# Optimization experiments

Measured on AMD Instinct MI355X. Metric: run time of the kernel, lower is better.

Reference implementation:

```python
import jax, jax.numpy as jnp
import numpy as np

D_MODEL = 1024
N_HEADS = 16
D_K = D_MODEL // N_HEADS


def setup_inputs() -> dict:
    key = jax.random.key(0)
    kx, kq, kk, kv, ko = jax.random.split(key, 5)
    scale = 1.0 / np.sqrt(D_MODEL)
    return {
        "x": jax.random.normal(kx, (2, 2048, D_MODEL), dtype=jnp.float32),
        "W_Q": jax.random.normal(kq, (D_MODEL, D_MODEL), dtype=jnp.float32) * scale,
        "W_K": jax.random.normal(kk, (D_MODEL, D_MODEL), dtype=jnp.float32) * scale,
        "W_V": jax.random.normal(kv, (D_MODEL, D_MODEL), dtype=jnp.float32) * scale,
        "W_O": jax.random.normal(ko, (D_MODEL, D_MODEL), dtype=jnp.float32) * scale,
    }


def reference(x, W_Q, W_K, W_V, W_O) -> jnp.ndarray:
    B, S, _ = x.shape
    # Projections; weights stored as (d_model, d_model), applied as x @ W (Linear weight transposed convention folded into init)
    def heads(w):
        return jnp.einsum('bsd,de->bse', x, w).reshape(B, S, N_HEADS, D_K).transpose(0, 2, 1, 3)
    Q, K, V = heads(W_Q), heads(W_K), heads(W_V)  # (B,H,S,d_k)
    scores = jnp.einsum('bhqd,bhkd->bhqk', Q, K) / jnp.sqrt(jnp.asarray(D_K, x.dtype))
    causal_mask = jnp.triu(jnp.ones((S, S), dtype=bool), k=1)  # True above diagonal
    scores = jnp.where(causal_mask[None, None], jnp.asarray(-jnp.inf, x.dtype), scores)
    attn = jax.nn.softmax(scores, axis=-1)
    out = jnp.einsum('bhqk,bhkd->bhqd', attn, V)  # (B,H,S,d_k)
    out = out.transpose(0, 2, 1, 3).reshape(B, S, N_HEADS * D_K)
    return jnp.einsum('bsd,de->bse', out, W_O)
```

## Files before the change

### kernel.cpp

```cpp
#include <hip/hip_runtime.h>

typedef unsigned short u16;
typedef unsigned int u32;
typedef __attribute__((ext_vector_type(8))) __bf16 bf16x8;
typedef __attribute__((ext_vector_type(2))) __bf16 bf16x2;
typedef __attribute__((ext_vector_type(4))) float f32x4;
typedef __attribute__((ext_vector_type(16))) float f32x16;
typedef __attribute__((ext_vector_type(4))) u32 u32x4;

__device__ inline u16 f2bf(float f) {
  unsigned u = __builtin_bit_cast(unsigned, f);
  u += 0x7FFFu + ((u >> 16) & 1u);
  return (u16)(u >> 16);
}

__device__ inline u32 packbf(float a, float b) {
  bf16x2 t;
  t[0] = (__bf16)a;
  t[1] = (__bf16)b;
  return __builtin_bit_cast(u32, t);
}

__device__ inline void async16(const void* g, void* l) {
  __builtin_amdgcn_global_load_lds((const __attribute__((address_space(1))) void*)g,
                                   (__attribute__((address_space(3))) void*)l, 16, 0, 0);
}

__global__ __launch_bounds__(256) void prep(const float* __restrict__ x, u16* __restrict__ xb,
                                            const float* __restrict__ W0,
                                            const float* __restrict__ W1,
                                            const float* __restrict__ W2,
                                            const float* __restrict__ W3,
                                            u16* __restrict__ WtQKV,
                                            u16* __restrict__ WtO) {
  const int z = blockIdx.z;
  if (z == 4) {
    const int base = (blockIdx.y * 32 + blockIdx.x) * 4 * 256 + threadIdx.x;
#pragma unroll
    for (int it = 0; it < 4; ++it) {
      const int i = base + it * 256;
      float4 v = ((const float4*)x)[i];
      ushort4 r;
      r.x = f2bf(v.x); r.y = f2bf(v.y); r.z = f2bf(v.z); r.w = f2bf(v.w);
      ((ushort4*)xb)[i] = r;
    }
    return;
  }
  __shared__ u16 tile[32][33];
  const float* W = (z == 0) ? W0 : (z == 1) ? W1 : (z == 2) ? W2 : W3;
  u16* Wt = (z < 3) ? (WtQKV + (size_t)z * 1024 * 1024) : WtO;
  const float s = (z == 0) ? 0.18033688011112042f : 1.0f;
  const int e0 = blockIdx.x * 32;
  const int d0 = blockIdx.y * 32;
  const int tx = threadIdx.x & 31;
  const int ty = threadIdx.x >> 5;
#pragma unroll
  for (int i = ty; i < 32; i += 8)
    tile[i][tx] = f2bf(W[(size_t)(d0 + i) * 1024 + e0 + tx] * s);
  __syncthreads();
#pragma unroll
  for (int i = ty; i < 32; i += 8)
    Wt[(size_t)(e0 + i) * 1024 + d0 + tx] = tile[tx][i];
}

template <int OUT_BF16, int FUSE_V>
__global__ __launch_bounds__(256) void gemm_bt(const u16* __restrict__ A,
                                               const u16* __restrict__ Bt,
                                               void* __restrict__ Cp,
                                               u16* __restrict__ Vtg,
                                               int M, int N, int K) {
  __shared__ __align__(16) u16 As[128 * 32];
  __shared__ __align__(16) u16 Bs[128 * 32];
  const int tid = threadIdx.x;
  const int lane = tid & 63;
  const int wave = tid >> 6;
  const int lr = lane & 15;
  const int lk = (lane >> 4) * 8;
  const int wm = (wave >> 1) * 64;
  const int wn = (wave & 1) * 64;

  const int flat = blockIdx.y * gridDim.x + blockIdx.x;
  const int chunk = (gridDim.x * gridDim.y) >> 3;
  const int nf = (flat & 7) * chunk + (flat >> 3);
  const int bm = (nf % gridDim.x) * 128;
  const int bn = (nf / gridDim.x) * 128;

  const int srow = lane >> 2;
  const int scol = (lane & 3) * 8;

  f32x4 acc[4][4] = {};

  for (int k0 = 0; k0 < K; k0 += 32) {
#pragma unroll
    for (int r = 0; r < 2; ++r) {
      const int chnk = r * 4 + wave;
      const int row = chnk * 16 + srow;
      async16(A + (size_t)(bm + row) * K + k0 + scol, &As[chnk * 512 + lane * 8]);
      async16(Bt + (size_t)(bn + row) * K + k0 + scol, &Bs[chnk * 512 + lane * 8]);
    }
    __syncthreads();
    bf16x8 a[4], b[4];
#pragma unroll
    for (int i = 0; i < 4; ++i) {
      a[i] = *(const bf16x8*)&As[(wm + i * 16 + lr) * 32 + lk];
      b[i] = *(const bf16x8*)&Bs[(wn + i * 16 + lr) * 32 + lk];
    }
#pragma unroll
    for (int mi = 0; mi < 4; ++mi)
#pragma unroll
      for (int ni = 0; ni < 4; ++ni)
        acc[mi][ni] = __builtin_amdgcn_mfma_f32_16x16x32_bf16(a[mi], b[ni], acc[mi][ni], 0, 0, 0);
    __syncthreads();
  }

#pragma unroll
  for (int mi = 0; mi < 4; ++mi) {
    const int row = bm + wm + mi * 16 + (lane >> 4) * 4;
#pragma unroll
    for (int ni = 0; ni < 4; ++ni) {
      const int col = bn + wn + ni * 16 + lr;
#pragma unroll
      for (int j = 0; j < 4; ++j) {
        if (OUT_BF16)
          ((u16*)Cp)[(size_t)(row + j) * N + col] = f2bf(acc[mi][ni][j]);
        else
          ((float*)Cp)[(size_t)(row + j) * N + col] = acc[mi][ni][j];
      }
      if (FUSE_V && col >= 2048) {
        const int bloc = row >> 11;
        const int s = row & 2047;
        const int sp = (s & ~12) | ((s & 4) << 1) | ((s & 8) >> 1);
        ushort4 v4;
        v4.x = f2bf(acc[mi][ni][0]);
        v4.y = f2bf(acc[mi][ni][1]);
        v4.z = f2bf(acc[mi][ni][2]);
        v4.w = f2bf(acc[mi][ni][3]);
        *(ushort4*)(Vtg + (size_t)(bloc * 1024 + (col - 2048)) * 2048 + sp) = v4;
      }
    }
  }
}

__global__ __launch_bounds__(256, 2) void attn_kernel(const u16* __restrict__ QKV,
                                                      const u16* __restrict__ Vtg,
                                                      u16* __restrict__ Opart,
                                                      float* __restrict__ Lpart) {
  constexpr int S = 2048, LD = 3072;
  constexpr float MFIX = 12.0f;
  __shared__ __align__(16) u16 Ks[2][64 * 64];
  __shared__ __align__(16) u16 Vs[2][64 * 64];

  const int flat = blockIdx.y * 16 + blockIdx.x;
  const int nf = (flat & 7) * 64 + (flat >> 3);
  const int xi = nf & 15;
  const int bh = nf >> 4;

  const int g = 7 - (xi >> 1);
  const int c = xi & 1;
  const int b = bh >> 4, h = bh & 15;
  const int tid = threadIdx.x, lane = tid & 63, w = tid >> 6;
  const int l31 = lane & 31, lh = lane >> 5;

  const int qbase = g * 256 + w * 64;
  const int ktlast = 4 * g + w;
  const int ktbeg = c * (2 * g + 2);
  const int ktend = (c + 1) * (2 * g + 2);

  bf16x8 qf[2][4];
#pragma unroll
  for (int qh = 0; qh < 2; ++qh) {
    const u16* qrow = QKV + (size_t)(b * S + qbase + qh * 32 + l31) * LD + h * 64;
#pragma unroll
    for (int cc = 0; cc < 4; ++cc) qf[qh][cc] = *(const bf16x8*)(qrow + cc * 16 + lh * 8);
  }

  const int c0 = tid, c1 = tid + 256;
  const int r0 = c0 >> 3, x0 = ((c0 & 7) ^ (r0 & 7)) << 3;
  const int r1 = c1 >> 3, x1 = ((c1 & 7) ^ (r1 & 7)) << 3;
  const u16* Kbase = QKV + (size_t)b * S * LD + 1024 + h * 64;
  const u16* Vbase = Vtg + (size_t)bh * 64 * 2048;

#define STAGE(buf, kt_)                                                          \
  do {                                                                           \
    async16(Kbase + (size_t)((kt_)*64 + r0) * LD + x0, &Ks[buf][c0 * 8]);        \
    async16(Kbase + (size_t)((kt_)*64 + r1) * LD + x1, &Ks[buf][c1 * 8]);        \
    async16(Vbase + (size_t)r0 * 2048 + (kt_)*64 + x0, &Vs[buf][c0 * 8]);        \
    async16(Vbase + (size_t)r1 * 2048 + (kt_)*64 + x1, &Vs[buf][c1 * 8]);        \
  } while (0)

  f32x16 o00 = {}, o01 = {}, o10 = {}, o11 = {};
  float l0 = 0.f, l1 = 0.f;

#define TREE16(dst, arr)                                                         \
  do {                                                                           \
    float v_[16];                                                                \
    _Pragma("unroll") for (int r_ = 0; r_ < 16; ++r_) v_[r_] = (arr)[r_];        \
    _Pragma("unroll") for (int s_ = 8; s_ >= 1; s_ >>= 1)                        \
      _Pragma("unroll") for (int r_ = 0; r_ < s_; ++r_) v_[r_] += v_[r_ + s_];   \
    dst += v_[0];                                                                \
  } while (0)

#define MAKE_PA(pa, pk, q4)                                                      \
  bf16x8 pa;                                                                     \
  {                                                                              \
    u32x4 wv_;                                                                   \
    wv_[0] = (pk)[(q4) + 0];                                                     \
    wv_[1] = (pk)[(q4) + 1];                                                     \
    wv_[2] = (pk)[(q4) + 2];                                                     \
    wv_[3] = (pk)[(q4) + 3];                                                     \
    pa = __builtin_bit_cast(bf16x8, wv_);                                        \
  }

  STAGE(0, ktbeg);

  int cur = 0;
  for (int kt = ktbeg; kt < ktend; ++kt) {
    if (kt + 1 < ktend) {
      STAGE(cur ^ 1, kt + 1);
      asm volatile("s_waitcnt vmcnt(4)" ::: "memory");
    } else {
      asm volatile("s_waitcnt vmcnt(0)" ::: "memory");
    }
    __builtin_amdgcn_s_barrier();
    __builtin_amdgcn_sched_barrier(0);

    const bool active = (kt <= ktlast);
    if (active) {
      const bool full = (kt < ktlast);
      const u16* ks = Ks[cur];
      const u16* vs = Vs[cur];

      f32x16 t00 = {}, t10 = {}, t01 = {}, t11 = {};
      __builtin_amdgcn_s_setprio(1);
#pragma unroll
      for (int cc = 0; cc < 4; ++cc) {
        const int ci = 2 * cc + lh;
        const bf16x8 kf0 = *(const bf16x8*)&ks[l31 * 64 + ((ci ^ (l31 & 7)) << 3)];
        const bf16x8 kf1 = *(const bf16x8*)&ks[(32 + l31) * 64 + ((ci ^ (l31 & 7)) << 3)];
        t00 = __builtin_amdgcn_mfma_f32_32x32x16_bf16(kf0, qf[0][cc], t00, 0, 0, 0);
        t01 = __builtin_amdgcn_mfma_f32_32x32x16_bf16(kf0, qf[1][cc], t01, 0, 0, 0);
        if (full) t10 = __builtin_amdgcn_mfma_f32_32x32x16_bf16(kf1, qf[0][cc], t10, 0, 0, 0);
        t11 = __builtin_amdgcn_mfma_f32_32x32x16_bf16(kf1, qf[1][cc], t11, 0, 0, 0);
      }
      __builtin_amdgcn_s_setprio(0);

      if (!full) {
#pragma unroll
        for (int r = 0; r < 16; ++r) {
          const int ko = (r & 3) + 8 * (r >> 2) + 4 * lh;
          if (ko > l31) { t00[r] = -3e38f; t11[r] = -3e38f; }
        }
      }

      u32 pk0[8], pk1[8];

#pragma unroll
      for (int r = 0; r < 16; ++r) t00[r] = exp2f(t00[r] - MFIX);
#pragma unroll
      for (int r = 0; r < 16; ++r) t01[r] = exp2f(t01[r] - MFIX);
      TREE16(l0, t00);
      TREE16(l1, t01);
#pragma unroll
      for (int j = 0; j < 8; ++j) {
        pk0[j] = packbf(t00[2 * j], t00[2 * j + 1]);
        pk1[j] = packbf(t01[2 * j], t01[2 * j + 1]);
      }
      __builtin_amdgcn_s_setprio(1);
#pragma unroll
      for (int kc = 0; kc < 2; ++kc) {
        const int q4 = kc * 4;
        MAKE_PA(pa0, pk0, q4)
        MAKE_PA(pa1, pk1, q4)
        const int ci = 2 * kc + lh;
        const bf16x8 vd0 = *(const bf16x8*)&vs[l31 * 64 + ((ci ^ (l31 & 7)) << 3)];
        const bf16x8 vd1 = *(const bf16x8*)&vs[(32 + l31) * 64 + ((ci ^ (l31 & 7)) << 3)];
        o00 = __builtin_amdgcn_mfma_f32_32x32x16_bf16(pa0, vd0, o00, 0, 0, 0);
        o01 = __builtin_amdgcn_mfma_f32_32x32x16_bf16(pa0, vd1, o01, 0, 0, 0);
        o10 = __builtin_amdgcn_mfma_f32_32x32x16_bf16(pa1, vd0, o10, 0, 0, 0);
        o11 = __builtin_amdgcn_mfma_f32_32x32x16_bf16(pa1, vd1, o11, 0, 0, 0);
      }
      __builtin_amdgcn_s_setprio(0);

      if (full) {
#pragma unroll
        for (int r = 0; r < 16; ++r) t10[r] = exp2f(t10[r] - MFIX);
        TREE16(l0, t10);
#pragma unroll
        for (int j = 0; j < 8; ++j) pk0[j] = packbf(t10[2 * j], t10[2 * j + 1]);
      }
#pragma unroll
      for (int r = 0; r < 16; ++r) t11[r] = exp2f(t11[r] - MFIX);
      TREE16(l1, t11);
#pragma unroll
      for (int j = 0; j < 8; ++j) pk1[j] = packbf(t11[2 * j], t11[2 * j + 1]);

      __builtin_amdgcn_s_setprio(1);
#pragma unroll
      for (int kc = 0; kc < 2; ++kc) {
        const int q4 = kc * 4;
        MAKE_PA(pa1, pk1, q4)
        const int ci = 2 * (kc + 2) + lh;
        const bf16x8 vd0 = *(const bf16x8*)&vs[l31 * 64 + ((ci ^ (l31 & 7)) << 3)];
        const bf16x8 vd1 = *(const bf16x8*)&vs[(32 + l31) * 64 + ((ci ^ (l31 & 7)) << 3)];
        if (full) {
          MAKE_PA(pa0, pk0, q4)
          o00 = __builtin_amdgcn_mfma_f32_32x32x16_bf16(pa0, vd0, o00, 0, 0, 0);
          o01 = __builtin_amdgcn_mfma_f32_32x32x16_bf16(pa0, vd1, o01, 0, 0, 0);
        }
        o10 = __builtin_amdgcn_mfma_f32_32x32x16_bf16(pa1, vd0, o10, 0, 0, 0);
        o11 = __builtin_amdgcn_mfma_f32_32x32x16_bf16(pa1, vd1, o11, 0, 0, 0);
      }
      __builtin_amdgcn_s_setprio(0);
    }

    asm volatile("s_waitcnt lgkmcnt(0)" ::: "memory");
    __builtin_amdgcn_s_barrier();
    cur ^= 1;
  }
#undef STAGE
#undef TREE16
#undef MAKE_PA

  const float l0t = l0 + __shfl_xor(l0, 32);
  const float l1t = l1 + __shfl_xor(l1, 32);
  u16* Oc = Opart + (size_t)c * 4096 * 1024;
#pragma unroll
  for (int r = 0; r < 16; ++r) {
    const int qo = (r & 3) + 8 * (r >> 2) + 4 * lh;
    u16* p0 = Oc + (size_t)(b * S + qbase + qo) * 1024 + h * 64 + l31;
    u16* p1 = p0 + (size_t)32 * 1024;
    p0[0] = f2bf(o00[r]);
    p0[32] = f2bf(o01[r]);
    p1[0] = f2bf(o10[r]);
    p1[32] = f2bf(o11[r]);
  }
  if (lh == 0) {
    Lpart[(size_t)c * 4096 * 16 + (size_t)(b * S + qbase + l31) * 16 + h] = l0t;
    Lpart[(size_t)c * 4096 * 16 + (size_t)(b * S + qbase + 32 + l31) * 16 + h] = l1t;
  }
}

__global__ __launch_bounds__(256) void combine(const u16* __restrict__ Opart,
                                               const float* __restrict__ Lpart,
                                               u16* __restrict__ Obuf) {
  const int i = blockIdx.x * 256 + threadIdx.x;
  const int row = i >> 7;
  const int cw = (i & 127) * 8;
  const int h = cw >> 6;
  const float l = Lpart[(size_t)row * 16 + h] + Lpart[(size_t)4096 * 16 + (size_t)row * 16 + h];
  const float inv = 1.0f / l;
  const bf16x8 a = *(const bf16x8*)(Opart + (size_t)row * 1024 + cw);
  const bf16x8 bq = *(const bf16x8*)(Opart + (size_t)4096 * 1024 + (size_t)row * 1024 + cw);
  u16 out[8];
#pragma unroll
  for (int j = 0; j < 8; ++j) out[j] = f2bf(((float)a[j] + (float)bq[j]) * inv);
  *(uint4*)(Obuf + (size_t)row * 1024 + cw) = *(uint4*)out;
}

extern "C" void kernel_launch(void* const* d_in, const int* in_sizes, int n_in,
                              void* d_out, int out_size, void* d_ws, size_t ws_size,
                              hipStream_t stream) {
  const float* x  = (const float*)d_in[0];
  const float* WQ = (const float*)d_in[1];
  const float* WK = (const float*)d_in[2];
  const float* WV = (const float*)d_in[3];
  const float* WO = (const float*)d_in[4];
  float* out = (float*)d_out;

  u16* xb    = (u16*)d_ws;
  u16* WtQKV = xb + (size_t)4096 * 1024;
  u16* WtO   = WtQKV + (size_t)3072 * 1024;
  u16* QKV   = WtO + (size_t)1024 * 1024;
  u16* Obuf  = QKV + (size_t)4096 * 3072;
  u16* Vtg   = Obuf + (size_t)4096 * 1024;
  u16* Opart = Vtg + (size_t)2048 * 2048;
  float* Lpart = (float*)(Opart + (size_t)2 * 4096 * 1024);

  prep<<<dim3(32, 32, 5), 256, 0, stream>>>(x, xb, WQ, WK, WV, WO, WtQKV, WtO);

  gemm_bt<1, 1><<<dim3(32, 24), 256, 0, stream>>>(xb, WtQKV, QKV, Vtg, 4096, 3072, 1024);
  attn_kernel<<<dim3(16, 32), 256, 0, stream>>>(QKV, Vtg, Opart, Lpart);
  combine<<<2048, 256, 0, stream>>>(Opart, Lpart, Obuf);
  gemm_bt<0, 0><<<dim3(32, 8), 256, 0, stream>>>(Obuf, WtO, out, nullptr, 4096, 1024, 1024);
}
```

Baseline: 138.2 us.

## Add 256x256-tile 8-wave QKV GEMM with split-K double buffering; fold softmax offset

Replaces the 128x128 QKV projection GEMM with a new 512-thread kernel using 256x256 output tiles, 64-wide K steps split into two 32-wide halves, double-buffered async LDS loads with swizzling, and interleaved A/B staging across barriers. The larger tile raises reuse per loaded byte and reduces block count to 192. The attention kernel also initialises score accumulators to -MFIX so the subtraction before exp2 is dropped. The cost is more registers and LDS per block, a grid that covers fewer blocks than there are CUs, and hardcoded shape constants.

After: 140.5 us. No clear change (+1.6%).

```diff
diff --git a/kernel.cpp b/kernel.cpp
--- a/kernel.cpp
+++ b/kernel.cpp
@@ -63,11 +63,136 @@
     Wt[(size_t)(e0 + i) * 1024 + d0 + tx] = tile[tx][i];
 }
 
-template <int OUT_BF16, int FUSE_V>
+__global__ __launch_bounds__(512, 2) void gemm8(const u16* __restrict__ A,
+                                                const u16* __restrict__ Bt,
+                                                u16* __restrict__ C,
+                                                u16* __restrict__ Vtg) {
+  constexpr int K = 1024, N = 3072, NT = 16;
+  __shared__ __align__(16) u16 Als[2][2][128 * 64];
+  __shared__ __align__(16) u16 Bls[2][2][128 * 64];
+
+  const int tid = threadIdx.x;
+  const int lane = tid & 63;
+  const int wid = tid >> 6;
+  const int wm = wid >> 2;
+  const int wn = wid & 3;
+  const int lr = lane & 15;
+  const int kc4 = lane >> 4;
+
+  const int flat = blockIdx.y * gridDim.x + blockIdx.x;
+  const int nf = (flat & 7) * 24 + (flat >> 3);
+  const int bm = (nf % 16) * 256;
+  const int bn = (nf / 16) * 256;
+
+  int srow[2], skof[2], sdst[2];
+#pragma unroll
+  for (int i = 0; i < 2; ++i) {
+    const int ch = tid + 512 * i;
+    const int R = ch >> 3, c = ch & 7;
+    const int cp = c ^ (R & 7);
+    srow[i] = 2 * R + (cp >> 2);
+    skof[i] = (cp & 3) * 8;
+    sdst[i] = ch * 8;
+  }
+
+#define STAGEH(LDSA, G, rowbase, o, kap, kt_)                                          \
+  do {                                                                                 \
+    _Pragma("unroll") for (int i_ = 0; i_ < 2; ++i_)                                   \
+      async16(G + (size_t)((rowbase) + srow[i_]) * K + (kt_)*64 + (kap)*32 + skof[i_], \
+              &LDSA[o][kap][sdst[i_]]);                                                \
+  } while (0)
+
+#define FRAG_OFF(r) ((((r) >> 1) * 8 + ((((r)&1) * 4 + kc4) ^ (((r) >> 1) & 7))) * 8)
+
+  f32x4 acc[8][4] = {};
+  bf16x8 af[4], bf[4];
+
+  STAGEH(Als, A, bm, 0, 0, 0);
+  STAGEH(Bls, Bt, bn, 0, 0, 0);
+  STAGEH(Als, A, bm, 0, 1, 0);
+  STAGEH(Bls, Bt, bn, 0, 1, 0);
+
+  for (int kt = 0; kt < NT; ++kt) {
+    const int s = kt & 1, o = s ^ 1;
+    const bool more = (kt + 1 < NT);
+
+#pragma unroll
+    for (int kk = 0; kk < 2; ++kk) {
+      if (more) STAGEH(Als, A, bm, o, kk, kt + 1);
+      if (more) {
+        asm volatile("s_waitcnt vmcnt(6)" ::: "memory");
+      } else if (kk == 0) {
+        asm volatile("s_waitcnt vmcnt(4)" ::: "memory");
+      } else {
+        asm volatile("s_waitcnt vmcnt(0)" ::: "memory");
+      }
+      __builtin_amdgcn_s_barrier();
+      __builtin_amdgcn_sched_barrier(0);
+
+#pragma unroll
+      for (int ni = 0; ni < 4; ++ni)
+        bf[ni] = *(const bf16x8*)&Bls[s][kk][FRAG_OFF(wn * 64 + ni * 16 + lr)];
+#pragma unroll
+      for (int mi = 0; mi < 4; ++mi)
+        af[mi] = *(const bf16x8*)&Als[s][kk][FRAG_OFF(wm * 128 + mi * 16 + lr)];
+      asm volatile("s_waitcnt lgkmcnt(0)" ::: "memory");
+      __builtin_amdgcn_sched_barrier(0);
+      __builtin_amdgcn_s_setprio(1);
+#pragma unroll
+      for (int mi = 0; mi < 4; ++mi)
+#pragma unroll
+        for (int ni = 0; ni < 4; ++ni)
+          acc[mi][ni] = __builtin_amdgcn_mfma_f32_16x16x32_bf16(af[mi], bf[ni], acc[mi][ni], 0, 0, 0);
+      __builtin_amdgcn_s_setprio(0);
+      __builtin_amdgcn_s_barrier();
+
+      if (more) STAGEH(Bls, Bt, bn, o, kk, kt + 1);
+#pragma unroll
+      for (int mi = 0; mi < 4; ++mi)
+        af[mi] = *(const bf16x8*)&Als[s][kk][FRAG_OFF(wm * 128 + (mi + 4) * 16 + lr)];
+      asm volatile("s_waitcnt lgkmcnt(0)" ::: "memory");
+      __builtin_amdgcn_sched_barrier(0);
+      __builtin_amdgcn_s_setprio(1);
+#pragma unroll
+      for (int mi = 0; mi < 4; ++mi)
+#pragma unroll
+        for (int ni = 0; ni < 4; ++ni)
+          acc[mi + 4][ni] = __builtin_amdgcn_mfma_f32_16x16x32_bf16(af[mi], bf[ni], acc[mi + 4][ni], 0, 0, 0);
+      __builtin_amdgcn_s_setprio(0);
+      __builtin_amdgcn_s_barrier();
+    }
+  }
+#undef STAGEH
+#undef FRAG_OFF
+
+#pragma unroll
+  for (int mi = 0; mi < 8; ++mi) {
+    const int row = bm + wm * 128 + mi * 16 + (lane >> 4) * 4;
+#pragma unroll
+    for (int ni = 0; ni < 4; ++ni) {
+      const int col = bn + wn * 64 + ni * 16 + lr;
+#pragma unroll
+      for (int j = 0; j < 4; ++j)
+        C[(size_t)(row + j) * N + col] = f2bf(acc[mi][ni][j]);
+      if (col >= 2048) {
+        const int bloc = row >> 11;
+        const int sidx = row & 2047;
+        const int sp = (sidx & ~12) | ((sidx & 4) << 1) | ((sidx & 8) >> 1);
+        ushort4 v4;
+        v4.x = f2bf(acc[mi][ni][0]);
+        v4.y = f2bf(acc[mi][ni][1]);
+        v4.z = f2bf(acc[mi][ni][2]);
+        v4.w = f2bf(acc[mi][ni][3]);
+        *(ushort4*)(Vtg + (size_t)(bloc * 1024 + (col - 2048)) * 2048 + sp) = v4;
+      }
+    }
+  }
+}
+
+template <int OUT_BF16>
 __global__ __launch_bounds__(256) void gemm_bt(const u16* __restrict__ A,
                                                const u16* __restrict__ Bt,
                                                void* __restrict__ Cp,
-                                               u16* __restrict__ Vtg,
                                                int M, int N, int K) {
   __shared__ __align__(16) u16 As[128 * 32];
   __shared__ __align__(16) u16 Bs[128 * 32];
@@ -126,17 +251,6 @@
         else
           ((float*)Cp)[(size_t)(row + j) * N + col] = acc[mi][ni][j];
       }
-      if (FUSE_V && col >= 2048) {
-        const int bloc = row >> 11;
-        const int s = row & 2047;
-        const int sp = (s & ~12) | ((s & 4) << 1) | ((s & 8) >> 1);
-        ushort4 v4;
-        v4.x = f2bf(acc[mi][ni][0]);
-        v4.y = f2bf(acc[mi][ni][1]);
-        v4.z = f2bf(acc[mi][ni][2]);
-        v4.w = f2bf(acc[mi][ni][3]);
-        *(ushort4*)(Vtg + (size_t)(bloc * 1024 + (col - 2048)) * 2048 + sp) = v4;
-      }
     }
   }
 }
@@ -230,7 +344,9 @@
       const u16* ks = Ks[cur];
       const u16* vs = Vs[cur];
 
-      f32x16 t00 = {}, t10 = {}, t01 = {}, t11 = {};
+      f32x16 t00, t10, t01, t11;
+#pragma unroll
+      for (int r = 0; r < 16; ++r) { t00[r] = -MFIX; t10[r] = -MFIX; t01[r] = -MFIX; t11[r] = -MFIX; }
       __builtin_amdgcn_s_setprio(1);
 #pragma unroll
       for (int cc = 0; cc < 4; ++cc) {
@@ -255,9 +371,9 @@
       u32 pk0[8], pk1[8];
 
 #pragma unroll
-      for (int r = 0; r < 16; ++r) t00[r] = exp2f(t00[r] - MFIX);
-#pragma unroll
-      for (int r = 0; r < 16; ++r) t01[r] = exp2f(t01[r] - MFIX);
+      for (int r = 0; r < 16; ++r) t00[r] = exp2f(t00[r]);
+#pragma unroll
+      for (int r = 0; r < 16; ++r) t01[r] = exp2f(t01[r]);
       TREE16(l0, t00);
       TREE16(l1, t01);
 #pragma unroll
@@ -283,13 +399,13 @@
 
       if (full) {
 #pragma unroll
-        for (int r = 0; r < 16; ++r) t10[r] = exp2f(t10[r] - MFIX);
+        for (int r = 0; r < 16; ++r) t10[r] = exp2f(t10[r]);
         TREE16(l0, t10);
 #pragma unroll
         for (int j = 0; j < 8; ++j) pk0[j] = packbf(t10[2 * j], t10[2 * j + 1]);
       }
 #pragma unroll
-      for (int r = 0; r < 16; ++r) t11[r] = exp2f(t11[r] - MFIX);
+      for (int r = 0; r < 16; ++r) t11[r] = exp2f(t11[r]);
       TREE16(l1, t11);
 #pragma unroll
       for (int j = 0; j < 8; ++j) pk1[j] = packbf(t11[2 * j], t11[2 * j + 1]);
@@ -378,8 +494,8 @@
 
   prep<<<dim3(32, 32, 5), 256, 0, stream>>>(x, xb, WQ, WK, WV, WO, WtQKV, WtO);
 
-  gemm_bt<1, 1><<<dim3(32, 24), 256, 0, stream>>>(xb, WtQKV, QKV, Vtg, 4096, 3072, 1024);
+  gemm8<<<dim3(16, 12), 512, 0, stream>>>(xb, WtQKV, QKV, Vtg);
   attn_kernel<<<dim3(16, 32), 256, 0, stream>>>(QKV, Vtg, Opart, Lpart);
   combine<<<2048, 256, 0, stream>>>(Opart, Lpart, Obuf);
-  gemm_bt<0, 0><<<dim3(32, 8), 256, 0, stream>>>(Obuf, WtO, out, nullptr, 4096, 1024, 1024);
-}
+  gemm_bt<0><<<dim3(32, 8), 256, 0, stream>>>(Obuf, WtO, out, 4096, 1024, 1024);
+}
```

## Fuse split-KV combine into output GEMM A-load and fold MFIX into accumulator init

Applied to the files above, without the earlier changes.

Drops the separate combine kernel. The output projection GEMM now reads both attention partial outputs and their row sums directly, normalises them and converts to bf16 while staging the A tile into LDS. This removes one launch and the Obuf round trip through memory. In exchange, every bn block repeats the combine work and the A loads become synchronous instead of async. Separately, the score accumulators start at -MFIX so the per-element subtraction before exp2 goes away.

After: 166.1 us. +20.2%, slower.

```diff
diff --git a/kernel.cpp b/kernel.cpp
--- a/kernel.cpp
+++ b/kernel.cpp
@@ -63,12 +63,11 @@
     Wt[(size_t)(e0 + i) * 1024 + d0 + tx] = tile[tx][i];
 }
 
-template <int OUT_BF16, int FUSE_V>
-__global__ __launch_bounds__(256) void gemm_bt(const u16* __restrict__ A,
-                                               const u16* __restrict__ Bt,
-                                               void* __restrict__ Cp,
-                                               u16* __restrict__ Vtg,
-                                               int M, int N, int K) {
+__global__ __launch_bounds__(256) void gemm_qkv(const u16* __restrict__ A,
+                                                const u16* __restrict__ Bt,
+                                                u16* __restrict__ C,
+                                                u16* __restrict__ Vtg) {
+  constexpr int K = 1024, N = 3072;
   __shared__ __align__(16) u16 As[128 * 32];
   __shared__ __align__(16) u16 Bs[128 * 32];
   const int tid = threadIdx.x;
@@ -120,13 +119,9 @@
     for (int ni = 0; ni < 4; ++ni) {
       const int col = bn + wn + ni * 16 + lr;
 #pragma unroll
-      for (int j = 0; j < 4; ++j) {
-        if (OUT_BF16)
-          ((u16*)Cp)[(size_t)(row + j) * N + col] = f2bf(acc[mi][ni][j]);
-        else
-          ((float*)Cp)[(size_t)(row + j) * N + col] = acc[mi][ni][j];
-      }
-      if (FUSE_V && col >= 2048) {
+      for (int j = 0; j < 4; ++j)
+        C[(size_t)(row + j) * N + col] = f2bf(acc[mi][ni][j]);
+      if (col >= 2048) {
         const int bloc = row >> 11;
         const int s = row & 2047;
         const int sp = (s & ~12) | ((s & 4) << 1) | ((s & 8) >> 1);
@@ -141,6 +136,76 @@
   }
 }
 
+__global__ __launch_bounds__(256) void gemm_out(const u16* __restrict__ Opart,
+                                                const float* __restrict__ Lpart,
+                                                const u16* __restrict__ Bt,
+                                                float* __restrict__ out) {
+  constexpr int K = 1024, N = 1024;
+  __shared__ __align__(16) u16 As[128 * 32];
+  __shared__ __align__(16) u16 Bs[128 * 32];
+  const int tid = threadIdx.x;
+  const int lane = tid & 63;
+  const int wave = tid >> 6;
+  const int lr = lane & 15;
+  const int lk = (lane >> 4) * 8;
+  const int wm = (wave >> 1) * 64;
+  const int wn = (wave & 1) * 64;
+
+  const int flat = blockIdx.y * gridDim.x + blockIdx.x;
+  const int chunk = (gridDim.x * gridDim.y) >> 3;
+  const int nf = (flat & 7) * chunk + (flat >> 3);
+  const int bm = (nf % gridDim.x) * 128;
+  const int bn = (nf / gridDim.x) * 128;
+
+  const int srow = lane >> 2;
+  const int scol = (lane & 3) * 8;
+
+  f32x4 acc[4][4] = {};
+
+  for (int k0 = 0; k0 < K; k0 += 32) {
+    const int hh = (k0 + scol) >> 6;
+#pragma unroll
+    for (int r = 0; r < 2; ++r) {
+      const int chnk = r * 4 + wave;
+      const int row = bm + chnk * 16 + srow;
+      const bf16x8 a0 = *(const bf16x8*)(Opart + (size_t)row * 1024 + k0 + scol);
+      const bf16x8 a1 = *(const bf16x8*)(Opart + (size_t)4096 * 1024 + (size_t)row * 1024 + k0 + scol);
+      const float inv = 1.0f / (Lpart[(size_t)row * 16 + hh] +
+                                Lpart[(size_t)4096 * 16 + (size_t)row * 16 + hh]);
+      u16 tmp[8];
+#pragma unroll
+      for (int j = 0; j < 8; ++j) tmp[j] = f2bf(((float)a0[j] + (float)a1[j]) * inv);
+      *(uint4*)&As[chnk * 512 + lane * 8] = *(uint4*)tmp;
+      async16(Bt + (size_t)(bn + chnk * 16 + srow) * K + k0 + scol, &Bs[chnk * 512 + lane * 8]);
+    }
+    __syncthreads();
+    bf16x8 a[4], b[4];
+#pragma unroll
+    for (int i = 0; i < 4; ++i) {
+      a[i] = *(const bf16x8*)&As[(wm + i * 16 + lr) * 32 + lk];
+      b[i] = *(const bf16x8*)&Bs[(wn + i * 16 + lr) * 32 + lk];
+    }
+#pragma unroll
+    for (int mi = 0; mi < 4; ++mi)
+#pragma unroll
+      for (int ni = 0; ni < 4; ++ni)
+        acc[mi][ni] = __builtin_amdgcn_mfma_f32_16x16x32_bf16(a[mi], b[ni], acc[mi][ni], 0, 0, 0);
+    __syncthreads();
+  }
+
+#pragma unroll
+  for (int mi = 0; mi < 4; ++mi) {
+    const int row = bm + wm + mi * 16 + (lane >> 4) * 4;
+#pragma unroll
+    for (int ni = 0; ni < 4; ++ni) {
+      const int col = bn + wn + ni * 16 + lr;
+#pragma unroll
+      for (int j = 0; j < 4; ++j)
+        out[(size_t)(row + j) * N + col] = acc[mi][ni][j];
+    }
+  }
+}
+
 __global__ __launch_bounds__(256, 2) void attn_kernel(const u16* __restrict__ QKV,
                                                       const u16* __restrict__ Vtg,
                                                       u16* __restrict__ Opart,
@@ -230,7 +295,9 @@
       const u16* ks = Ks[cur];
       const u16* vs = Vs[cur];
 
-      f32x16 t00 = {}, t10 = {}, t01 = {}, t11 = {};
+      f32x16 t00, t10, t01, t11;
+#pragma unroll
+      for (int r = 0; r < 16; ++r) { t00[r] = -MFIX; t10[r] = -MFIX; t01[r] = -MFIX; t11[r] = -MFIX; }
       __builtin_amdgcn_s_setprio(1);
 #pragma unroll
       for (int cc = 0; cc < 4; ++cc) {
@@ -255,9 +322,9 @@
       u32 pk0[8], pk1[8];
 
 #pragma unroll
-      for (int r = 0; r < 16; ++r) t00[r] = exp2f(t00[r] - MFIX);
-#pragma unroll
-      for (int r = 0; r < 16; ++r) t01[r] = exp2f(t01[r] - MFIX);
+      for (int r = 0; r < 16; ++r) t00[r] = exp2f(t00[r]);
+#pragma unroll
+      for (int r = 0; r < 16; ++r) t01[r] = exp2f(t01[r]);
       TREE16(l0, t00);
       TREE16(l1, t01);
 #pragma unroll
@@ -283,13 +350,13 @@
 
       if (full) {
 #pragma unroll
-        for (int r = 0; r < 16; ++r) t10[r] = exp2f(t10[r] - MFIX);
+        for (int r = 0; r < 16; ++r) t10[r] = exp2f(t10[r]);
         TREE16(l0, t10);
 #pragma unroll
         for (int j = 0; j < 8; ++j) pk0[j] = packbf(t10[2 * j], t10[2 * j + 1]);
       }
 #pragma unroll
-      for (int r = 0; r < 16; ++r) t11[r] = exp2f(t11[r] - MFIX);
+      for (int r = 0; r < 16; ++r) t11[r] = exp2f(t11[r]);
       TREE16(l1, t11);
 #pragma unroll
       for (int j = 0; j < 8; ++j) pk1[j] = packbf(t11[2 * j], t11[2 * j + 1]);
@@ -340,23 +407,6 @@
   }
 }
 
-__global__ __launch_bounds__(256) void combine(const u16* __restrict__ Opart,
-                                               const float* __restrict__ Lpart,
-                                               u16* __restrict__ Obuf) {
-  const int i = blockIdx.x * 256 + threadIdx.x;
-  const int row = i >> 7;
-  const int cw = (i & 127) * 8;
-  const int h = cw >> 6;
-  const float l = Lpart[(size_t)row * 16 + h] + Lpart[(size_t)4096 * 16 + (size_t)row * 16 + h];
-  const float inv = 1.0f / l;
-  const bf16x8 a = *(const bf16x8*)(Opart + (size_t)row * 1024 + cw);
-  const bf16x8 bq = *(const bf16x8*)(Opart + (size_t)4096 * 1024 + (size_t)row * 1024 + cw);
-  u16 out[8];
-#pragma unroll
-  for (int j = 0; j < 8; ++j) out[j] = f2bf(((float)a[j] + (float)bq[j]) * inv);
-  *(uint4*)(Obuf + (size_t)row * 1024 + cw) = *(uint4*)out;
-}
-
 extern "C" void kernel_launch(void* const* d_in, const int* in_sizes, int n_in,
                               void* d_out, int out_size, void* d_ws, size_t ws_size,
                               hipStream_t stream) {
@@ -371,15 +421,13 @@
   u16* WtQKV = xb + (size_t)4096 * 1024;
   u16* WtO   = WtQKV + (size_t)3072 * 1024;
   u16* QKV   = WtO + (size_t)1024 * 1024;
-  u16* Obuf  = QKV + (size_t)4096 * 3072;
-  u16* Vtg   = Obuf + (size_t)4096 * 1024;
+  u16* Vtg   = QKV + (size_t)4096 * 3072;
   u16* Opart = Vtg + (size_t)2048 * 2048;
   float* Lpart = (float*)(Opart + (size_t)2 * 4096 * 1024);
 
   prep<<<dim3(32, 32, 5), 256, 0, stream>>>(x, xb, WQ, WK, WV, WO, WtQKV, WtO);
 
-  gemm_bt<1, 1><<<dim3(32, 24), 256, 0, stream>>>(xb, WtQKV, QKV, Vtg, 4096, 3072, 1024);
+  gemm_qkv<<<dim3(32, 24), 256, 0, stream>>>(xb, WtQKV, QKV, Vtg);
   attn_kernel<<<dim3(16, 32), 256, 0, stream>>>(QKV, Vtg, Opart, Lpart);
-  combine<<<2048, 256, 0, stream>>>(Opart, Lpart, Obuf);
-  gemm_bt<0, 0><<<dim3(32, 8), 256, 0, stream>>>(Obuf, WtO, out, nullptr, 4096, 1024, 1024);
-}
+  gemm_out<<<dim3(32, 8), 256, 0, stream>>>(Opart, Lpart, WtO, out);
+}
```
